# Optimization experiments

Measured on AMD Instinct MI355X. Metric: run time of the kernel, lower is better.

The kernel has to match this reference:

```python
import jax, jax.numpy as jnp
import numpy as np

VOCAB, VEC, HID, ATT, DOM, B, S = 50000, 300, 256, 500, 16, 64, 128


def _gru_scan(gi_all, h0, Whh, bhh):
    # gi_all: [S,B,3H] precomputed input projections; returns hs: [S,B,H]
    def step(h, gi):
        gh = h @ Whh.T + bhh
        i_r, i_z, i_n = jnp.split(gi, 3, axis=-1)
        h_r, h_z, h_n = jnp.split(gh, 3, axis=-1)
        r = jax.nn.sigmoid(i_r + h_r)
        zg = jax.nn.sigmoid(i_z + h_z)
        n = jnp.tanh(i_n + r * h_n)
        h_new = (1.0 - zg) * n + zg * h
        return h_new, h_new
    _, hs = jax.lax.scan(step, h0, gi_all)
    return hs


def setup_inputs() -> dict:
    key = jax.random.key(0)
    ks = jax.random.split(key, 16)
    def xavier(k, shape):
        fan_in, fan_out = shape[-1], shape[0]
        std = float(np.sqrt(2.0 / (fan_in + fan_out)))
        return jax.random.normal(k, shape, dtype=jnp.float32) * std
    inp = {
        'x': jax.random.randint(ks[0], (B, S), 0, VOCAB),
        'z': jax.random.randint(ks[1], (B,), 0, DOM),
        'emb': jax.random.normal(ks[2], (VOCAB, VEC), dtype=jnp.float32) * 0.1,
        'Wih_f': xavier(ks[3], (3 * HID, VEC)),
        'Whh_f': xavier(ks[4], (3 * HID, HID)),
        'bih_f': jnp.zeros((3 * HID,), jnp.float32),
        'bhh_f': jnp.zeros((3 * HID,), jnp.float32),
        'Wih_b': xavier(ks[5], (3 * HID, VEC)),
        'Whh_b': xavier(ks[6], (3 * HID, HID)),
        'bih_b': jnp.zeros((3 * HID,), jnp.float32),
        'bhh_b': jnp.zeros((3 * HID,), jnp.float32),
        'att_fc_W': xavier(ks[7], (ATT, 2 * HID)),
        'att_fc_b': jnp.zeros((ATT,), jnp.float32),
        'att_weight': xavier(ks[8], (DOM, ATT)),
        'fc_W': xavier(ks[9], (2, 2 * HID)),
        'fc_b': jnp.zeros((2,), jnp.float32),
    }
    return inp


def reference(x, z, emb, Wih_f, Whh_f, bih_f, bhh_f, Wih_b, Whh_b, bih_b, bhh_b,
              att_fc_W, att_fc_b, att_weight, fc_W, fc_b):
    xe = emb[x]                              # [B,S,VEC]
    xs = jnp.transpose(xe, (1, 0, 2))        # [S,B,VEC] (seq-major like torch GRU)
    h0 = jnp.zeros((x.shape[0], HID), jnp.float32)
    gi_f = jnp.einsum('sbv,gv->sbg', xs, Wih_f) + bih_f
    hs_f = _gru_scan(gi_f, h0, Whh_f, bhh_f)                       # [S,B,H]
    gi_b = jnp.einsum('sbv,gv->sbg', xs[::-1], Wih_b) + bih_b
    hs_b = _gru_scan(gi_b, h0, Whh_b, bhh_b)[::-1]                 # [S,B,H]
    h = jnp.transpose(jnp.concatenate([hs_f, hs_b], axis=-1), (1, 0, 2))  # [B,S,2H]
    hr = jnp.tanh(jnp.einsum('bsh,ah->bsa', h, att_fc_W) + att_fc_b)      # [B,S,ATT]
    # batched gather of per-domain attention vector, then per-row dot
    u = jnp.einsum('bsa,ba->bs', hr, att_weight[z])                        # [B,S]
    att = jax.nn.softmax(u, axis=1)                                        # [B,S]
    pooled = jnp.einsum('bsh,bs->bh', h, att)                              # [B,2H]
    # dropout is identity in eval mode
    return pooled @ fc_W.T + fc_b                                          # [B,2]
```

## Files before the change

kernel.cpp:

```cpp
#include <hip/hip_runtime.h>
#include <math.h>

#define VEC   300
#define HID   256
#define ATT   500
#define NB    64
#define NS    128
#define G3    768
#define GIC   1536
#define H2    512
#define KP    320

typedef _Float16 half1;
typedef _Float16 h2_t  __attribute__((ext_vector_type(2)));
typedef _Float16 f16x8 __attribute__((ext_vector_type(8)));
typedef float    f32x4 __attribute__((ext_vector_type(4)));

struct __align__(16) H8 { h2_t a, b, c, d; };

#if __has_builtin(__builtin_amdgcn_exp2f)
#define EXP2F(x) __builtin_amdgcn_exp2f(x)
#else
#define EXP2F(x) exp2f(x)
#endif
#if __has_builtin(__builtin_amdgcn_rcpf)
#define RCPF(x) __builtin_amdgcn_rcpf(x)
#else
#define RCPF(x) (1.0f/(x))
#endif

__device__ __forceinline__ float sigm(float x){ return RCPF(1.f + EXP2F(-1.44269504f*x)); }
__device__ __forceinline__ float tanh_fast(float x){ return 1.f - 2.f*RCPF(1.f + EXP2F(2.88539008f*x)); }

#if __has_builtin(__builtin_amdgcn_fdot2)
#define FDOT(w,h,acc) __builtin_amdgcn_fdot2((w),(h),(acc),false)
#else
#define FDOT(w,h,acc) ((acc) + (float)(w).x*(float)(h).x + (float)(w).y*(float)(h).y)
#endif

__global__ __launch_bounds__(256) void k_prep2(const float* __restrict__ Wf,
                       const float* __restrict__ Wb, h2_t* __restrict__ Wpk){
  int o = blockIdx.x*256 + threadIdx.x;
  int t = o & 511;
  int rest = o >> 9;
  int j = rest % 3;
  int p = (rest/3) & 63;
  int dir = rest / 192;
  int u = (t >> 6)*32 + (t & 31);
  int ks = (t >> 5) & 1;
  const float* W = dir ? Wb : Wf;
  int k0 = ks*128 + 2*p;
  h2_t w;
  w.x = (half1)W[(j*HID+u)*HID + k0];
  w.y = (half1)W[(j*HID+u)*HID + k0 + 1];
  Wpk[o] = w;
}

__global__ __launch_bounds__(256) void k_prepA(const float* __restrict__ afW,
                       half1* __restrict__ afW16){
  int o = blockIdx.x*256 + threadIdx.x;
  int n = o >> 9, k = o & 511;
  afW16[o] = (half1)((n < ATT) ? afW[n*H2 + k] : 0.f);
}

__global__ __launch_bounds__(256) void k_prepXW(const int* __restrict__ x,
      const float* __restrict__ emb,
      const float* __restrict__ Wf, const float* __restrict__ Wb,
      h2_t* __restrict__ xe16, h2_t* __restrict__ W16){
  int o = blockIdx.x*256 + threadIdx.x;
  const int NXE = 8192*160;
  if (o < NXE) {
    int i = o / 160, kp = o - 160*(o/160);
    int k0 = kp*2;
    int s = i >> 6, b = i & 63;
    h2_t v; v.x = (half1)0.f; v.y = (half1)0.f;
    if (k0 < VEC) {
      const float* e = &emb[(long)x[b*NS + s]*VEC];
      v.x = (half1)e[k0];
      v.y = (half1)((k0+1 < VEC) ? e[k0+1] : 0.f);
    }
    xe16[(long)i*160 + kp] = v;
  } else {
    int o2 = o - NXE;
    if (o2 >= 1536*160) return;
    int g = o2 / 160, kp = o2 - 160*(o2/160);
    int k0 = kp*2;
    h2_t v; v.x = (half1)0.f; v.y = (half1)0.f;
    if (k0 < VEC) {
      const float* wr = (g < G3) ? &Wf[(long)g*VEC] : &Wb[(long)(g-G3)*VEC];
      v.x = (half1)wr[k0];
      v.y = (half1)((k0+1 < VEC) ? wr[k0+1] : 0.f);
    }
    W16[(long)g*160 + kp] = v;
  }
}

__global__ __launch_bounds__(256)
__attribute__((amdgpu_waves_per_eu(4, 4)))
void k_gi16f(const half1* __restrict__ xe16, const half1* __restrict__ W16,
      const float* __restrict__ bf, const float* __restrict__ bb,
      float* __restrict__ gi){
  const int t = threadIdx.x;
  const int row0 = blockIdx.x * 128;
  const int col0 = blockIdx.y * 128;
  const int lane = t & 63, wid = t >> 6;
  const int wr = wid >> 1, wc = wid & 1;
  const int l15 = lane & 15, lk = lane >> 4;

  f32x4 acc[4][4];
#pragma unroll
  for (int i = 0; i < 4; ++i)
#pragma unroll
    for (int j = 0; j < 4; ++j) acc[i][j] = (f32x4){0.f,0.f,0.f,0.f};

#pragma unroll 1
  for (int ks = 0; ks < 10; ++ks) {
    f16x8 af[4], bfq[4];
#pragma unroll
    for (int i = 0; i < 4; ++i) {
      int row = row0 + wr*64 + i*16 + l15;
      af[i] = *reinterpret_cast<const f16x8*>(&xe16[(long)row*KP + ks*32 + lk*8]);
    }
#pragma unroll
    for (int j = 0; j < 4; ++j) {
      int g = col0 + wc*64 + j*16 + l15;
      bfq[j] = *reinterpret_cast<const f16x8*>(&W16[(long)g*KP + ks*32 + lk*8]);
    }
#pragma unroll
    for (int i = 0; i < 4; ++i)
#pragma unroll
      for (int j = 0; j < 4; ++j)
        acc[i][j] = __builtin_amdgcn_mfma_f32_16x16x32_f16(af[i], bfq[j], acc[i][j], 0, 0, 0);
  }

#pragma unroll
  for (int j = 0; j < 4; ++j) {
    int gcol = col0 + wc*64 + j*16 + l15;
    float bj = (gcol < G3) ? bf[gcol] : bb[gcol - G3];
#pragma unroll
    for (int i = 0; i < 4; ++i) {
      int grow0 = row0 + wr*64 + i*16 + lk*4;
#pragma unroll
      for (int q = 0; q < 4; ++q)
        gi[(long)(grow0 + q)*GIC + gcol] = acc[i][j][q] + bj;
    }
  }
}

#define DECL12(X,g,UNUSED) h2_t X##g##a0,X##g##a1,X##g##a2, X##g##b0,X##g##b1,X##g##b2, \
                                X##g##c0,X##g##c1,X##g##c2, X##g##d0,X##g##d1,X##g##d2;
#define LOAD12(X,g,PB) \
  X##g##a0=wp[(((PB)+4*(g)+0)*3+0)*512]; X##g##a1=wp[(((PB)+4*(g)+0)*3+1)*512]; X##g##a2=wp[(((PB)+4*(g)+0)*3+2)*512]; \
  X##g##b0=wp[(((PB)+4*(g)+1)*3+0)*512]; X##g##b1=wp[(((PB)+4*(g)+1)*3+1)*512]; X##g##b2=wp[(((PB)+4*(g)+1)*3+2)*512]; \
  X##g##c0=wp[(((PB)+4*(g)+2)*3+0)*512]; X##g##c1=wp[(((PB)+4*(g)+2)*3+1)*512]; X##g##c2=wp[(((PB)+4*(g)+2)*3+2)*512]; \
  X##g##d0=wp[(((PB)+4*(g)+3)*3+0)*512]; X##g##d1=wp[(((PB)+4*(g)+3)*3+1)*512]; X##g##d2=wp[(((PB)+4*(g)+3)*3+2)*512];
#define FMA12(X,g,BOFF) { \
  H8 hv = *reinterpret_cast<const H8*>(&hr[(BOFF) + (g)*8]); \
  a0=FDOT(X##g##a0,hv.a,a0); a1=FDOT(X##g##a1,hv.a,a1); a2=FDOT(X##g##a2,hv.a,a2); \
  a0=FDOT(X##g##b0,hv.b,a0); a1=FDOT(X##g##b1,hv.b,a1); a2=FDOT(X##g##b2,hv.b,a2); \
  a0=FDOT(X##g##c0,hv.c,a0); a1=FDOT(X##g##c1,hv.c,a1); a2=FDOT(X##g##c2,hv.c,a2); \
  a0=FDOT(X##g##d0,hv.d,a0); a1=FDOT(X##g##d1,hv.d,a1); a2=FDOT(X##g##d2,hv.d,a2); }
#define GRP8(M,X,A2) M(X,0,A2) M(X,1,A2) M(X,2,A2) M(X,3,A2) M(X,4,A2) M(X,5,A2) M(X,6,A2) M(X,7,A2)

__global__ __launch_bounds__(512)
__attribute__((amdgpu_waves_per_eu(2, 2)))
void k_scan_reg6(const float* __restrict__ gi,
     const h2_t* __restrict__ Wpk,
     const float* __restrict__ bhf, const float* __restrict__ bhb,
     float* __restrict__ hseq){
  __shared__ __align__(16) half1 hist[129*256];
  const int t    = threadIdx.x;
  const int lane = t & 63;
  const int ul   = lane & 31;
  const int ks   = lane >> 5;
  const int w    = t >> 6;
  const int u    = w*32 + ul;
  const int ks128 = ks * 128;
  const int dir  = blockIdx.x & 1;
  const int b    = blockIdx.x >> 1;
  const float* bhh = dir ? bhb : bhf;
  const h2_t* wp = Wpk + (long)dir*98304 + t;

  GRP8(DECL12, A, 0)
  GRP8(DECL12, B, 0)
  GRP8(LOAD12, A, 0)
  GRP8(LOAD12, B, 32)

  const bool fin = (ks == 0);
  float bh0=0.f, bh1=0.f, bh2=0.f;
  if (fin) { bh0 = bhh[u]; bh1 = bhh[HID+u]; bh2 = bhh[2*HID+u]; }
  if (t < 256) hist[t] = (half1)0.f;
  float hprev = 0.f;

  const long gstep = dir ? -(long)NB*GIC : (long)NB*GIC;
  long gbase = ((long)(dir ? (NS-1) : 0)*NB + b)*GIC + dir*G3 + u;
  __syncthreads();

#pragma unroll 1
  for (int tt = 0; tt < NS; ++tt) {
    float i0=0.f, i1=0.f, i2=0.f;
    if (fin) {
      i0 = gi[gbase]; i1 = gi[gbase+HID]; i2 = gi[gbase+2*HID];
    }
    const half1* hr = &hist[tt*256 + ks128];
    float a0=0.f, a1=0.f, a2=0.f;
    GRP8(FMA12, A, 0)
    GRP8(FMA12, B, 64)
    a0 += __shfl_xor(a0, 32, 64);
    a1 += __shfl_xor(a1, 32, 64);
    a2 += __shfl_xor(a2, 32, 64);
    if (fin) {
      float g0 = bh0 + a0;
      float g1 = bh1 + a1;
      float g2 = bh2 + a2;
      float r  = sigm(i0 + g0);
      float zg = sigm(i1 + g1);
      float n  = tanh_fast(i2 + r*g2);
      float hn = (1.f - zg)*n + zg*hprev;
      hprev = hn;
      hist[(tt+1)*256 + u] = (half1)hn;
    }
    gbase += gstep;
    __syncthreads();
  }

#pragma unroll 1
  for (int it = 0; it < 16; ++it) {
    int idx = it*512 + t;
    int ttr = idx >> 6;
    int c4  = (idx & 63) * 4;
    int s   = dir ? (NS-1-ttr) : ttr;
    h2_t p0 = *reinterpret_cast<const h2_t*>(&hist[(ttr+1)*256 + c4]);
    h2_t p1 = *reinterpret_cast<const h2_t*>(&hist[(ttr+1)*256 + c4 + 2]);
    float4 v; v.x = (float)p0.x; v.y = (float)p0.y; v.z = (float)p1.x; v.w = (float)p1.y;
    *reinterpret_cast<float4*>(&hseq[((long)b*NS + s)*H2 + dir*HID + c4]) = v;
  }
}

__global__ __launch_bounds__(256)
__attribute__((amdgpu_waves_per_eu(4, 4)))
void k_att1_mfma(const float* __restrict__ hseq, const half1* __restrict__ afW16,
    const float* __restrict__ afb, const float* __restrict__ attw,
    const int* __restrict__ z, float* __restrict__ ub){
  __shared__ half1 Ah[32*520];
  __shared__ float red[4*32];
  const int t  = threadIdx.x;
  const int b  = blockIdx.x;
  const int s0 = blockIdx.y * 32;
  const int lane = t & 63, w = t >> 6;
  const int l15 = lane & 15, lk = lane >> 4;

#pragma unroll
  for (int l = 0; l < 64; ++l) {
    int idx = l*256 + t;
    int sl = idx >> 9, c = idx & 511;
    Ah[sl*520 + c] = (half1)hseq[((long)b*NS + s0 + sl)*H2 + c];
  }
  __syncthreads();

  f32x4 acc[2][8];
#pragma unroll
  for (int i = 0; i < 2; ++i)
#pragma unroll
    for (int j = 0; j < 8; ++j) acc[i][j] = (f32x4){0.f,0.f,0.f,0.f};

#pragma unroll 2
  for (int ksn = 0; ksn < 16; ++ksn) {
    f16x8 af[2];
#pragma unroll
    for (int mt = 0; mt < 2; ++mt)
      af[mt] = *reinterpret_cast<const f16x8*>(&Ah[(mt*16 + l15)*520 + ksn*32 + lk*8]);
#pragma unroll
    for (int nt = 0; nt < 8; ++nt) {
      int n = w*128 + nt*16 + l15;
      f16x8 bf = *reinterpret_cast<const f16x8*>(&afW16[(long)n*512 + ksn*32 + lk*8]);
#pragma unroll
      for (int mt = 0; mt < 2; ++mt)
        acc[mt][nt] = __builtin_amdgcn_mfma_f32_16x16x32_f16(af[mt], bf, acc[mt][nt], 0, 0, 0);
    }
  }

  float us[8];
#pragma unroll
  for (int i = 0; i < 8; ++i) us[i] = 0.f;
  const int zb = z[b];
#pragma unroll
  for (int nt = 0; nt < 8; ++nt) {
    int n = w*128 + nt*16 + l15;
    float ab = (n < ATT) ? afb[n] : 0.f;
    float aw = (n < ATT) ? attw[zb*ATT + n] : 0.f;
#pragma unroll
    for (int mt = 0; mt < 2; ++mt)
#pragma unroll
      for (int q = 0; q < 4; ++q)
        us[mt*4+q] += tanh_fast(acc[mt][nt][q] + ab) * aw;
  }
#pragma unroll
  for (int off = 1; off < 16; off <<= 1)
#pragma unroll
    for (int i = 0; i < 8; ++i) us[i] += __shfl_xor(us[i], off, 64);
  if (l15 == 0) {
#pragma unroll
    for (int i = 0; i < 8; ++i) {
      int row = (i >> 2)*16 + lk*4 + (i & 3);
      red[w*32 + row] = us[i];
    }
  }
  __syncthreads();
  if (t < 32)
    ub[b*NS + s0 + t] = red[t] + red[32+t] + red[64+t] + red[96+t];
}

__global__ __launch_bounds__(256) void k_att2(const float* __restrict__ hseq,
   const float* __restrict__ ub, const float* __restrict__ fcW,
   const float* __restrict__ fcb, float* __restrict__ out){
  __shared__ float att[NS];
  __shared__ float red[256];
  __shared__ float pool[H2];
  const int t = threadIdx.x, b = blockIdx.x;
  float v = (t < NS) ? ub[b*NS + t] : -3.4e38f;
  red[t] = v; __syncthreads();
  for (int off = 128; off >= 1; off >>= 1) {
    if (t < off) red[t] = fmaxf(red[t], red[t+off]);
    __syncthreads();
  }
  float mx = red[0]; __syncthreads();
  float e = (t < NS) ? EXP2F(1.44269504f*(v - mx)) : 0.f;
  red[t] = e; __syncthreads();
  for (int off = 128; off >= 1; off >>= 1) {
    if (t < off) red[t] += red[t+off];
    __syncthreads();
  }
  float sm = red[0]; __syncthreads();
  if (t < NS) att[t] = e / sm;
  __syncthreads();
#pragma unroll
  for (int rep = 0; rep < 2; ++rep) {
    int c = rep*256 + t;
    float acc = 0.f;
#pragma unroll 4
    for (int s = 0; s < NS; ++s) acc += att[s] * hseq[((long)b*NS + s)*H2 + c];
    pool[c] = acc;
  }
  __syncthreads();
  for (int j = 0; j < 2; ++j) {
    float p = pool[t]*fcW[j*H2+t] + pool[t+256]*fcW[j*H2+t+256];
    red[t] = p; __syncthreads();
    for (int off = 128; off >= 1; off >>= 1) {
      if (t < off) red[t] += red[t+off];
      __syncthreads();
    }
    if (t == 0) out[b*2+j] = red[0] + fcb[j];
    __syncthreads();
  }
}

extern "C" void kernel_launch(void* const* d_in, const int* in_sizes, int n_in,
                              void* d_out, int out_size, void* d_ws, size_t ws_size,
                              hipStream_t stream) {
  const int*   x     = (const int*)  d_in[0];
  const int*   z     = (const int*)  d_in[1];
  const float* emb   = (const float*)d_in[2];
  const float* Wih_f = (const float*)d_in[3];
  const float* Whh_f = (const float*)d_in[4];
  const float* bih_f = (const float*)d_in[5];
  const float* bhh_f = (const float*)d_in[6];
  const float* Wih_b = (const float*)d_in[7];
  const float* Whh_b = (const float*)d_in[8];
  const float* bih_b = (const float*)d_in[9];
  const float* bhh_b = (const float*)d_in[10];
  const float* afW   = (const float*)d_in[11];
  const float* afb   = (const float*)d_in[12];
  const float* attw  = (const float*)d_in[13];
  const float* fcW   = (const float*)d_in[14];
  const float* fcb   = (const float*)d_in[15];

  float* ws    = (float*)d_ws;
  h2_t*  Wpk   = (h2_t*)ws;
  half1* afW16 = (half1*)(ws + 196608);
  float* giW   = ws   + 196608 + 131072;
  float* hseq  = giW  + 12582912;
  float* ubuf  = hseq + 4194304;
  h2_t*  xe16  = (h2_t*)hseq;
  h2_t*  W16   = (h2_t*)(hseq + 1310720);

  k_prep2 <<<dim3(768),  dim3(256), 0, stream>>>(Whh_f, Whh_b, Wpk);
  k_prepA <<<dim3(1024), dim3(256), 0, stream>>>(afW, afW16);
  k_prepXW<<<dim3(6080), dim3(256), 0, stream>>>(x, emb, Wih_f, Wih_b, xe16, W16);
  k_gi16f <<<dim3(64,12), dim3(256), 0, stream>>>((const half1*)xe16, (const half1*)W16,
                                                  bih_f, bih_b, giW);
  k_scan_reg6<<<dim3(128), dim3(512), 0, stream>>>(giW, Wpk, bhh_f, bhh_b, hseq);
  k_att1_mfma<<<dim3(64,4), dim3(256), 0, stream>>>(hseq, afW16, afb, attw, z, ubuf);
  k_att2<<<dim3(64), dim3(256), 0, stream>>>(hseq, ubuf, fcW, fcb, (float*)d_out);
}
```

Baseline: 235.3 us.

## Remap GRU scan to two units per lane with 4-way K split; fuse prep kernels

The recurrent scan kernel now has each lane own two hidden units and a quarter of the K range, instead of one unit and half of K. Each hidden-state LDS read is therefore reused across six dot products rather than three. Reduction becomes a two-stage cross-lane shuffle, and the history buffer is padded to 288 halfs per row with 72-element segments to avoid LDS bank conflicts. The three preprocessing kernels are merged into one launch to cut launch overhead. The trade-off is extra shuffles per step and a new weight-packing layout that must match the scan indexing.

```diff
diff --git a/kernel.cpp b/kernel.cpp
--- a/kernel.cpp
+++ b/kernel.cpp
@@ -38,38 +38,45 @@
 #define FDOT(w,h,acc) ((acc) + (float)(w).x*(float)(h).x + (float)(w).y*(float)(h).y)
 #endif
 
-__global__ __launch_bounds__(256) void k_prep2(const float* __restrict__ Wf,
-                       const float* __restrict__ Wb, h2_t* __restrict__ Wpk){
-  int o = blockIdx.x*256 + threadIdx.x;
-  int t = o & 511;
-  int rest = o >> 9;
-  int j = rest % 3;
-  int p = (rest/3) & 63;
-  int dir = rest / 192;
-  int u = (t >> 6)*32 + (t & 31);
-  int ks = (t >> 5) & 1;
-  const float* W = dir ? Wb : Wf;
-  int k0 = ks*128 + 2*p;
-  h2_t w;
-  w.x = (half1)W[(j*HID+u)*HID + k0];
-  w.y = (half1)W[(j*HID+u)*HID + k0 + 1];
-  Wpk[o] = w;
-}
-
-__global__ __launch_bounds__(256) void k_prepA(const float* __restrict__ afW,
-                       half1* __restrict__ afW16){
-  int o = blockIdx.x*256 + threadIdx.x;
-  int n = o >> 9, k = o & 511;
-  afW16[o] = (half1)((n < ATT) ? afW[n*H2 + k] : 0.f);
-}
-
-__global__ __launch_bounds__(256) void k_prepXW(const int* __restrict__ x,
+#define N_WPK 196608
+#define N_AFW 262144
+#define N_XE  1310720
+#define N_W16 245760
+__global__ __launch_bounds__(256) void k_prep_all(const int* __restrict__ x,
       const float* __restrict__ emb,
-      const float* __restrict__ Wf, const float* __restrict__ Wb,
+      const float* __restrict__ Wih_f, const float* __restrict__ Wih_b,
+      const float* __restrict__ Whh_f, const float* __restrict__ Whh_b,
+      const float* __restrict__ afW,
+      h2_t* __restrict__ Wpk, half1* __restrict__ afW16,
       h2_t* __restrict__ xe16, h2_t* __restrict__ W16){
   int o = blockIdx.x*256 + threadIdx.x;
-  const int NXE = 8192*160;
-  if (o < NXE) {
+  if (o < N_WPK) {
+    int t = o & 511;
+    int rest = o >> 9;
+    int dir = rest / 192;
+    int r2  = rest - dir*192;
+    int p   = r2 / 6;
+    int r3  = r2 - p*6;
+    int uu  = r3 / 3;
+    int j   = r3 - uu*3;
+    int ul = t & 15, ks = (t >> 4) & 3, w = t >> 6;
+    int u = w*32 + ul*2 + uu;
+    const float* W = dir ? Whh_b : Whh_f;
+    int k0 = ks*64 + 2*p;
+    h2_t wv;
+    wv.x = (half1)W[(j*HID+u)*HID + k0];
+    wv.y = (half1)W[(j*HID+u)*HID + k0 + 1];
+    Wpk[o] = wv;
+    return;
+  }
+  o -= N_WPK;
+  if (o < N_AFW) {
+    int n = o >> 9, k = o & 511;
+    afW16[o] = (half1)((n < ATT) ? afW[n*H2 + k] : 0.f);
+    return;
+  }
+  o -= N_AFW;
+  if (o < N_XE) {
     int i = o / 160, kp = o - 160*(o/160);
     int k0 = kp*2;
     int s = i >> 6, b = i & 63;
@@ -80,14 +87,15 @@
       v.y = (half1)((k0+1 < VEC) ? e[k0+1] : 0.f);
     }
     xe16[(long)i*160 + kp] = v;
-  } else {
-    int o2 = o - NXE;
-    if (o2 >= 1536*160) return;
-    int g = o2 / 160, kp = o2 - 160*(o2/160);
+    return;
+  }
+  o -= N_XE;
+  if (o < N_W16) {
+    int g = o / 160, kp = o - 160*(o/160);
     int k0 = kp*2;
     h2_t v; v.x = (half1)0.f; v.y = (half1)0.f;
     if (k0 < VEC) {
-      const float* wr = (g < G3) ? &Wf[(long)g*VEC] : &Wb[(long)(g-G3)*VEC];
+      const float* wr = (g < G3) ? &Wih_f[(long)g*VEC] : &Wih_b[(long)(g-G3)*VEC];
       v.x = (half1)wr[k0];
       v.y = (half1)((k0+1 < VEC) ? wr[k0+1] : 0.f);
     }
@@ -147,78 +155,85 @@
   }
 }
 
-#define DECL12(X,g,UNUSED) h2_t X##g##a0,X##g##a1,X##g##a2, X##g##b0,X##g##b1,X##g##b2, \
-                                X##g##c0,X##g##c1,X##g##c2, X##g##d0,X##g##d1,X##g##d2;
-#define LOAD12(X,g,PB) \
-  X##g##a0=wp[(((PB)+4*(g)+0)*3+0)*512]; X##g##a1=wp[(((PB)+4*(g)+0)*3+1)*512]; X##g##a2=wp[(((PB)+4*(g)+0)*3+2)*512]; \
-  X##g##b0=wp[(((PB)+4*(g)+1)*3+0)*512]; X##g##b1=wp[(((PB)+4*(g)+1)*3+1)*512]; X##g##b2=wp[(((PB)+4*(g)+1)*3+2)*512]; \
-  X##g##c0=wp[(((PB)+4*(g)+2)*3+0)*512]; X##g##c1=wp[(((PB)+4*(g)+2)*3+1)*512]; X##g##c2=wp[(((PB)+4*(g)+2)*3+2)*512]; \
-  X##g##d0=wp[(((PB)+4*(g)+3)*3+0)*512]; X##g##d1=wp[(((PB)+4*(g)+3)*3+1)*512]; X##g##d2=wp[(((PB)+4*(g)+3)*3+2)*512];
-#define FMA12(X,g,BOFF) { \
-  H8 hv = *reinterpret_cast<const H8*>(&hr[(BOFF) + (g)*8]); \
-  a0=FDOT(X##g##a0,hv.a,a0); a1=FDOT(X##g##a1,hv.a,a1); a2=FDOT(X##g##a2,hv.a,a2); \
-  a0=FDOT(X##g##b0,hv.b,a0); a1=FDOT(X##g##b1,hv.b,a1); a2=FDOT(X##g##b2,hv.b,a2); \
-  a0=FDOT(X##g##c0,hv.c,a0); a1=FDOT(X##g##c1,hv.c,a1); a2=FDOT(X##g##c2,hv.c,a2); \
-  a0=FDOT(X##g##d0,hv.d,a0); a1=FDOT(X##g##d1,hv.d,a1); a2=FDOT(X##g##d2,hv.d,a2); }
-#define GRP8(M,X,A2) M(X,0,A2) M(X,1,A2) M(X,2,A2) M(X,3,A2) M(X,4,A2) M(X,5,A2) M(X,6,A2) M(X,7,A2)
+#define D6(g,e) h2_t W##g##e##00,W##g##e##01,W##g##e##02,W##g##e##10,W##g##e##11,W##g##e##12;
+#define DECL24(g) D6(g,a) D6(g,b) D6(g,c) D6(g,d)
+#define L6(g,e,p) \
+  W##g##e##00=wp[((p)*6+0)*512]; W##g##e##01=wp[((p)*6+1)*512]; W##g##e##02=wp[((p)*6+2)*512]; \
+  W##g##e##10=wp[((p)*6+3)*512]; W##g##e##11=wp[((p)*6+4)*512]; W##g##e##12=wp[((p)*6+5)*512];
+#define LOAD24(g) L6(g,a,4*(g)+0) L6(g,b,4*(g)+1) L6(g,c,4*(g)+2) L6(g,d,4*(g)+3)
+#define F6(g,e,HE) \
+  b0a0=FDOT(W##g##e##00,(HE),b0a0); b0a1=FDOT(W##g##e##01,(HE),b0a1); b0a2=FDOT(W##g##e##02,(HE),b0a2); \
+  b1a0=FDOT(W##g##e##10,(HE),b1a0); b1a1=FDOT(W##g##e##11,(HE),b1a1); b1a2=FDOT(W##g##e##12,(HE),b1a2);
+#define FMA24(g) { H8 hv = *reinterpret_cast<const H8*>(&hr[(g)*8]); \
+  F6(g,a,hv.a) F6(g,b,hv.b) F6(g,c,hv.c) F6(g,d,hv.d) }
+#define GRP8X(M) M(0) M(1) M(2) M(3) M(4) M(5) M(6) M(7)
 
 __global__ __launch_bounds__(512)
 __attribute__((amdgpu_waves_per_eu(2, 2)))
-void k_scan_reg6(const float* __restrict__ gi,
+void k_scan_reg9(const float* __restrict__ gi,
      const h2_t* __restrict__ Wpk,
      const float* __restrict__ bhf, const float* __restrict__ bhb,
      float* __restrict__ hseq){
-  __shared__ __align__(16) half1 hist[129*256];
+  __shared__ __align__(16) half1 hist[129*288];
   const int t    = threadIdx.x;
   const int lane = t & 63;
-  const int ul   = lane & 31;
-  const int ks   = lane >> 5;
+  const int ul   = lane & 15;
+  const int ks   = lane >> 4;
   const int w    = t >> 6;
-  const int u    = w*32 + ul;
-  const int ks128 = ks * 128;
+  const int u0   = w*32 + ul*2;
   const int dir  = blockIdx.x & 1;
   const int b    = blockIdx.x >> 1;
   const float* bhh = dir ? bhb : bhf;
   const h2_t* wp = Wpk + (long)dir*98304 + t;
 
-  GRP8(DECL12, A, 0)
-  GRP8(DECL12, B, 0)
-  GRP8(LOAD12, A, 0)
-  GRP8(LOAD12, B, 32)
+  GRP8X(DECL24)
+  GRP8X(LOAD24)
 
   const bool fin = (ks == 0);
-  float bh0=0.f, bh1=0.f, bh2=0.f;
-  if (fin) { bh0 = bhh[u]; bh1 = bhh[HID+u]; bh2 = bhh[2*HID+u]; }
-  if (t < 256) hist[t] = (half1)0.f;
-  float hprev = 0.f;
+  float bh00=0.f, bh01=0.f, bh10=0.f, bh11=0.f, bh20=0.f, bh21=0.f;
+  if (fin) {
+    float2 v0 = *reinterpret_cast<const float2*>(&bhh[u0]);
+    float2 v1 = *reinterpret_cast<const float2*>(&bhh[HID+u0]);
+    float2 v2 = *reinterpret_cast<const float2*>(&bhh[2*HID+u0]);
+    bh00 = v0.x; bh01 = v0.y; bh10 = v1.x; bh11 = v1.y; bh20 = v2.x; bh21 = v2.y;
+  }
+  if (t < 288) hist[t] = (half1)0.f;
+  float hprev0 = 0.f, hprev1 = 0.f;
 
   const long gstep = dir ? -(long)NB*GIC : (long)NB*GIC;
-  long gbase = ((long)(dir ? (NS-1) : 0)*NB + b)*GIC + dir*G3 + u;
+  long gbase = ((long)(dir ? (NS-1) : 0)*NB + b)*GIC + dir*G3 + u0;
   __syncthreads();
 
 #pragma unroll 1
   for (int tt = 0; tt < NS; ++tt) {
-    float i0=0.f, i1=0.f, i2=0.f;
+    float i00=0.f,i01=0.f,i10=0.f,i11=0.f,i20=0.f,i21=0.f;
     if (fin) {
-      i0 = gi[gbase]; i1 = gi[gbase+HID]; i2 = gi[gbase+2*HID];
-    }
-    const half1* hr = &hist[tt*256 + ks128];
-    float a0=0.f, a1=0.f, a2=0.f;
-    GRP8(FMA12, A, 0)
-    GRP8(FMA12, B, 64)
-    a0 += __shfl_xor(a0, 32, 64);
-    a1 += __shfl_xor(a1, 32, 64);
-    a2 += __shfl_xor(a2, 32, 64);
+      float2 v0 = *reinterpret_cast<const float2*>(&gi[gbase]);
+      float2 v1 = *reinterpret_cast<const float2*>(&gi[gbase+HID]);
+      float2 v2 = *reinterpret_cast<const float2*>(&gi[gbase+2*HID]);
+      i00 = v0.x; i01 = v0.y; i10 = v1.x; i11 = v1.y; i20 = v2.x; i21 = v2.y;
+    }
+    const half1* hr = &hist[tt*288 + ks*72];
+    float b0a0=0.f,b0a1=0.f,b0a2=0.f, b1a0=0.f,b1a1=0.f,b1a2=0.f;
+    GRP8X(FMA24)
+    b0a0 += __shfl_xor(b0a0, 16, 64); b0a0 += __shfl_xor(b0a0, 32, 64);
+    b0a1 += __shfl_xor(b0a1, 16, 64); b0a1 += __shfl_xor(b0a1, 32, 64);
+    b0a2 += __shfl_xor(b0a2, 16, 64); b0a2 += __shfl_xor(b0a2, 32, 64);
+    b1a0 += __shfl_xor(b1a0, 16, 64); b1a0 += __shfl_xor(b1a0, 32, 64);
+    b1a1 += __shfl_xor(b1a1, 16, 64); b1a1 += __shfl_xor(b1a1, 32, 64);
+    b1a2 += __shfl_xor(b1a2, 16, 64); b1a2 += __shfl_xor(b1a2, 32, 64);
     if (fin) {
-      float g0 = bh0 + a0;
-      float g1 = bh1 + a1;
-      float g2 = bh2 + a2;
-      float r  = sigm(i0 + g0);
-      float zg = sigm(i1 + g1);
-      float n  = tanh_fast(i2 + r*g2);
-      float hn = (1.f - zg)*n + zg*hprev;
-      hprev = hn;
-      hist[(tt+1)*256 + u] = (half1)hn;
+      float r0  = sigm(i00 + bh00 + b0a0);
+      float z0  = sigm(i10 + bh10 + b0a1);
+      float n0  = tanh_fast(i20 + bh20 + r0*b0a2);
+      float hn0 = (1.f - z0)*n0 + z0*hprev0;
+      float r1  = sigm(i01 + bh01 + b1a0);
+      float z1  = sigm(i11 + bh11 + b1a1);
+      float n1  = tanh_fast(i21 + bh21 + r1*b1a2);
+      float hn1 = (1.f - z1)*n1 + z1*hprev1;
+      hprev0 = hn0; hprev1 = hn1;
+      h2_t hw; hw.x = (half1)hn0; hw.y = (half1)hn1;
+      *reinterpret_cast<h2_t*>(&hist[(tt+1)*288 + (u0 >> 6)*72 + (u0 & 63)]) = hw;
     }
     gbase += gstep;
     __syncthreads();
@@ -230,8 +245,9 @@
     int ttr = idx >> 6;
     int c4  = (idx & 63) * 4;
     int s   = dir ? (NS-1-ttr) : ttr;
-    h2_t p0 = *reinterpret_cast<const h2_t*>(&hist[(ttr+1)*256 + c4]);
-    h2_t p1 = *reinterpret_cast<const h2_t*>(&hist[(ttr+1)*256 + c4 + 2]);
+    int base = (ttr+1)*288 + (c4 >> 6)*72 + (c4 & 63);
+    h2_t p0 = *reinterpret_cast<const h2_t*>(&hist[base]);
+    h2_t p1 = *reinterpret_cast<const h2_t*>(&hist[base + 2]);
     float4 v; v.x = (float)p0.x; v.y = (float)p0.y; v.z = (float)p1.x; v.w = (float)p1.y;
     *reinterpret_cast<float4*>(&hseq[((long)b*NS + s)*H2 + dir*HID + c4]) = v;
   }
@@ -384,12 +400,12 @@
   h2_t*  xe16  = (h2_t*)hseq;
   h2_t*  W16   = (h2_t*)(hseq + 1310720);
 
-  k_prep2 <<<dim3(768),  dim3(256), 0, stream>>>(Whh_f, Whh_b, Wpk);
-  k_prepA <<<dim3(1024), dim3(256), 0, stream>>>(afW, afW16);
-  k_prepXW<<<dim3(6080), dim3(256), 0, stream>>>(x, emb, Wih_f, Wih_b, xe16, W16);
+  const int prep_total = N_WPK + N_AFW + N_XE + N_W16;
+  k_prep_all<<<dim3((prep_total + 255)/256), dim3(256), 0, stream>>>(
+      x, emb, Wih_f, Wih_b, Whh_f, Whh_b, afW, Wpk, afW16, xe16, W16);
   k_gi16f <<<dim3(64,12), dim3(256), 0, stream>>>((const half1*)xe16, (const half1*)W16,
                                                   bih_f, bih_b, giW);
-  k_scan_reg6<<<dim3(128), dim3(512), 0, stream>>>(giW, Wpk, bhh_f, bhh_b, hseq);
+  k_scan_reg9<<<dim3(128), dim3(512), 0, stream>>>(giW, Wpk, bhh_f, bhh_b, hseq);
   k_att1_mfma<<<dim3(64,4), dim3(256), 0, stream>>>(hseq, afW16, afb, attw, z, ubuf);
   k_att2<<<dim3(64), dim3(256), 0, stream>>>(hseq, ubuf, fcW, fcb, (float*)d_out);
 }
```

New measurement: 254.0 us. 1.08x slower.
